# Kernel tuning notes

Measured on AMD Instinct MI355X. Metric: run time of the kernel, lower is better.

The kernel has to match this reference:

```python
import jax, jax.numpy as jnp
import numpy as np

N = 100000   # nodes
E = 1600000  # edges
G = 64       # graphs in batch
C = 8        # num_classes
H = 128      # hidden dim


def _lin(k, out_f, in_f):
    return jax.random.normal(k, (out_f, in_f), jnp.float32) * (1.0 / np.sqrt(in_f))


def setup_inputs() -> dict:
    key = jax.random.key(0)
    ks = jax.random.split(key, 16)
    x = jax.random.normal(ks[0], (N, 5), jnp.float32)
    edge_index = jax.random.randint(ks[1], (2, E), 0, N)
    batch = jnp.sort(jax.random.randint(ks[2], (N,), 0, G))
    exinfo = jax.random.normal(ks[3], (G, 10), jnp.float32)
    return {
        "x": x, "edge_index": edge_index, "batch": batch, "exinfo": exinfo,
        # GraphConv1: 3 -> 128 (PyG GraphConv: lin_root(x) + lin_rel(scatter_add(x_j)))
        "Wroot1": _lin(ks[4], H, 3), "Wrel1": _lin(ks[5], H, 3), "brel1": jnp.zeros((H,), jnp.float32),
        # GraphConv2: 128 -> 128
        "Wroot2": _lin(ks[6], H, H), "Wrel2": _lin(ks[7], H, H), "brel2": jnp.zeros((H,), jnp.float32),
        # MLP head
        "W1": _lin(ks[8], 64, 2 * H + 10), "b1": jnp.zeros((64,), jnp.float32),
        "W2": _lin(ks[9], 32, 64), "b2": jnp.zeros((32,), jnp.float32),
        "W3": _lin(ks[10], C, 32), "b3": jnp.zeros((C,), jnp.float32),
    }


def _graph_conv(x, src, dst, Wroot, Wrel, brel):
    # PyG GraphConv (aggr='add'): out_i = Wrel @ sum_{j->i} x_j + brel + Wroot @ x_i
    agg = jax.ops.segment_sum(x[src], dst, num_segments=x.shape[0])  # [N, F]
    return agg @ Wrel.T + brel + x @ Wroot.T


def reference(x, edge_index, batch, exinfo,
              Wroot1, Wrel1, brel1, Wroot2, Wrel2, brel2,
              W1, b1, W2, b2, W3, b3):
    xs = x[:, 2:5]                              # data.x[:, 2:5]
    src, dst = edge_index[0], edge_index[1]
    x1 = jax.nn.relu(_graph_conv(xs, src, dst, Wroot1, Wrel1, brel1))   # [N, 128]
    x2 = jax.nn.relu(_graph_conv(x1, src, dst, Wroot2, Wrel2, brel2))   # [N, 128]
    h = jnp.concatenate([x1, x2], axis=-1)      # [N, 256]
    g = jax.ops.segment_max(h, batch, num_segments=G)  # global max pool [G, 256]
    g = jnp.concatenate([g, exinfo], axis=-1)   # [G, 266]
    g = jax.nn.relu(g @ W1.T + b1)
    g = jax.nn.relu(g @ W2.T + b2)
    return jax.nn.log_softmax(g @ W3.T + b3, axis=-1)
```

## Files before the change

### kernel.cpp

```cpp
#include <hip/hip_runtime.h>

#define N_NODES 100000
#define N_EDGES 1600000
#define NG 64
#define NC 8
#define HD 128

#define BUCKET_SHIFT 8
#define NB ((N_NODES + 255) >> 8)
#define NCHUNK 256
#define EPC (N_EDGES / NCHUNK)

typedef __attribute__((ext_vector_type(8))) __bf16 bf16x8;
typedef __attribute__((ext_vector_type(4))) float f32x4;
typedef __attribute__((ext_vector_type(2))) float f32x2;


__global__ void hist_init_k(const int* __restrict__ dst, int* __restrict__ hist,
                            const float* __restrict__ x, const float* __restrict__ Wrel2,
                            const float* __restrict__ Wroot2, float4* __restrict__ xs4,
                            __bf16* __restrict__ Wc, unsigned int* __restrict__ g) {
  int t = threadIdx.x;
  if (blockIdx.x < NCHUNK) {
    __shared__ int lh[NB];
    int c = blockIdx.x;
    for (int b = t; b < NB; b += 256) lh[b] = 0;
    __syncthreads();
    int e0 = c * EPC;
    for (int i = t; i < EPC; i += 256) atomicAdd(&lh[dst[e0 + i] >> BUCKET_SHIFT], 1);
    __syncthreads();
    for (int b = t; b < NB; b += 256) hist[c * NB + b] = lh[b];
  } else {
    int i = (blockIdx.x - NCHUNK) * 256 + t;
    if (i < 64 * 256) g[i] = 0u;
    if (i < 32768) {
      int h = i >> 8, k = i & 255;
      float v = (k < 128) ? Wrel2[h * 128 + k] : Wroot2[h * 128 + (k - 128)];
      Wc[i] = (__bf16)v;
    }
    if (i < N_NODES) {
      const float* xp = x + (size_t)i * 5;
      xs4[i] = make_float4(xp[2], xp[3], xp[4], 0.f);
    }
  }
}


__launch_bounds__(512)
__global__ void sum_scan_k(const int* __restrict__ hist, int* __restrict__ bucket_base,
                           int* __restrict__ row_ptr) {
  __shared__ int sm[512];
  int t = threadIdx.x;
  int s = 0;
  if (t < NB) {
#pragma unroll 8
    for (int c = 0; c < NCHUNK; c++) s += hist[c * NB + t];
  }
  sm[t] = s;
  __syncthreads();
  for (int off = 1; off < 512; off <<= 1) {
    int v = (t >= off) ? sm[t - off] : 0;
    __syncthreads();
    sm[t] += v;
    __syncthreads();
  }
  if (t < NB) bucket_base[t] = sm[t] - s;
  if (t == 0) { bucket_base[NB] = N_EDGES; row_ptr[N_NODES] = N_EDGES; }
}

__global__ void chunk_scan_k(int* __restrict__ hist, const int* __restrict__ bucket_base) {
  int b = blockIdx.x, lane = threadIdx.x;
  int carry = bucket_base[b];
#pragma unroll
  for (int it = 0; it < NCHUNK / 64; it++) {
    int c = it * 64 + lane;
    int v = hist[c * NB + b];
    int s = v;
#pragma unroll
    for (int off = 1; off < 64; off <<= 1) {
      int u = __shfl_up(s, off);
      if (lane >= off) s += u;
    }
    hist[c * NB + b] = carry + s - v;
    carry += __shfl(s, 63);
  }
}

__global__ void scatter_k(const int* __restrict__ src, const int* __restrict__ dst,
                          const int* __restrict__ hist, unsigned int* __restrict__ pairs) {
  __shared__ int loff[NB];
  int c = blockIdx.x, t = threadIdx.x;
  for (int b = t; b < NB; b += 256) loff[b] = hist[c * NB + b];
  __syncthreads();
  int e0 = c * EPC;
  for (int i = t; i < EPC; i += 256) {
    int d = dst[e0 + i], s = src[e0 + i];
    int pos = atomicAdd(&loff[d >> BUCKET_SHIFT], 1);
    pairs[pos] = ((unsigned int)s << 8) | (unsigned int)(d & 255);
  }
}

__global__ void bucket_csr_k(const unsigned int* __restrict__ pairs,
                             const int* __restrict__ bucket_base,
                             int* __restrict__ row_ptr, int* __restrict__ csr) {
  __shared__ int cnt[256];
  __shared__ int start[256];
  __shared__ int wsum[4];
  int b = blockIdx.x, t = threadIdx.x, lane = t & 63, wid = t >> 6;
  int nb0 = b << BUCKET_SHIFT;
  int beg = bucket_base[b], end = bucket_base[b + 1];
  cnt[t] = 0;
  __syncthreads();
  for (int i = beg + t; i < end; i += 256) atomicAdd(&cnt[pairs[i] & 255u], 1);
  __syncthreads();
  int v = cnt[t];
  int s = v;
#pragma unroll
  for (int off = 1; off < 64; off <<= 1) {
    int u = __shfl_up(s, off);
    if (lane >= off) s += u;
  }
  if (lane == 63) wsum[wid] = s;
  __syncthreads();
  if (t == 0) {
    int a = 0;
    for (int j = 0; j < 4; j++) { int x = wsum[j]; wsum[j] = a; a += x; }
  }
  __syncthreads();
  int excl = wsum[wid] + s - v;
  start[t] = excl;
  if (nb0 + t < N_NODES) row_ptr[nb0 + t] = beg + excl;
  cnt[t] = 0;
  __syncthreads();
  for (int i = beg + t; i < end; i += 256) {
    unsigned int p = pairs[i];
    int li = p & 255u;
    int pos = beg + start[li] + atomicAdd(&cnt[li], 1);
    csr[pos] = (int)(p >> 8);
  }
}


__global__ void conv1_k(const float4* __restrict__ xs4, const int* __restrict__ row_ptr,
                        const int* __restrict__ csr, const float* __restrict__ Wroot1,
                        const float* __restrict__ Wrel1, const float* __restrict__ brel1,
                        __bf16* __restrict__ xcat) {
  int node = blockIdx.x * 4 + (threadIdx.x >> 6);
  if (node >= N_NODES) return;
  int lane = threadIdx.x & 63;
  int beg = row_ptr[node], end = row_ptr[node + 1];
  float a0 = 0.f, a1 = 0.f, a2 = 0.f;
  for (int e = beg + lane; e < end; e += 64) {
    float4 v = xs4[csr[e]];
    a0 += v.x; a1 += v.y; a2 += v.z;
  }
#pragma unroll
  for (int m = 1; m < 64; m <<= 1) {
    a0 += __shfl_xor(a0, m);
    a1 += __shfl_xor(a1, m);
    a2 += __shfl_xor(a2, m);
  }
  float4 rv = xs4[node];
  __bf16* orow = xcat + (size_t)node * 256 + 128;
#pragma unroll
  for (int hh = 0; hh < 2; hh++) {
    int h = lane + hh * 64;
    float v = brel1[h]
            + a0 * Wrel1[h * 3 + 0] + a1 * Wrel1[h * 3 + 1] + a2 * Wrel1[h * 3 + 2]
            + rv.x * Wroot1[h * 3 + 0] + rv.y * Wroot1[h * 3 + 1] + rv.z * Wroot1[h * 3 + 2];
    orow[h] = (__bf16)fmaxf(v, 0.f);
  }
}


#define LDROW(s) (*((const uint4*)(xcat + (size_t)(s) * 256 + 128) + f))
#define ACC8(u) \
  acc2[0] += (f32x2){__uint_as_float((u).x << 16), __uint_as_float((u).x & 0xffff0000u)}; \
  acc2[1] += (f32x2){__uint_as_float((u).y << 16), __uint_as_float((u).y & 0xffff0000u)}; \
  acc2[2] += (f32x2){__uint_as_float((u).z << 16), __uint_as_float((u).z & 0xffff0000u)}; \
  acc2[3] += (f32x2){__uint_as_float((u).w << 16), __uint_as_float((u).w & 0xffff0000u)};

__global__ void agg2_k(const int* __restrict__ row_ptr, const int* __restrict__ csr,
                       __bf16* xcat) {
  int node = blockIdx.x * 4 + (threadIdx.x >> 6);
  if (node >= N_NODES) return;
  int lane = threadIdx.x & 63;
  int g = lane >> 4, f = lane & 15;
  int beg = row_ptr[node], end = row_ptr[node + 1];
  int deg = end - beg;
  int idx = (lane < deg) ? csr[beg + lane] : 0;
  f32x2 acc2[4];
#pragma unroll
  for (int k = 0; k < 4; k++) acc2[k] = (f32x2){0.f, 0.f};
  int dmain = deg < 64 ? deg : 64;
  int j = 0;
  for (; j + 16 <= dmain; j += 16) {
    int s0 = __shfl(idx, j + g);
    int s1 = __shfl(idx, j + 4 + g);
    int s2 = __shfl(idx, j + 8 + g);
    int s3 = __shfl(idx, j + 12 + g);
    uint4 u0 = LDROW(s0);
    uint4 u1 = LDROW(s1);
    uint4 u2 = LDROW(s2);
    uint4 u3 = LDROW(s3);
    ACC8(u0) ACC8(u1) ACC8(u2) ACC8(u3)
  }
  if (j + 8 <= dmain) {
    int s0 = __shfl(idx, j + g);
    int s1 = __shfl(idx, j + 4 + g);
    uint4 u0 = LDROW(s0);
    uint4 u1 = LDROW(s1);
    ACC8(u0) ACC8(u1)
    j += 8;
  }
  if (j + 4 <= dmain) {
    int s0 = __shfl(idx, j + g);
    uint4 u0 = LDROW(s0);
    ACC8(u0)
    j += 4;
  }
  {
    int rem = dmain - j;
    int s0 = __shfl(idx, j + (g < rem ? g : 0));
    if (g < rem) {
      uint4 u0 = LDROW(s0);
      ACC8(u0)
    }
  }
  for (int e = beg + 64; e < end; e += 4) {
    int m = end - e;
    int s0 = csr[e + (g < m ? g : 0)];
    if (g < m) {
      uint4 u0 = LDROW(s0);
      ACC8(u0)
    }
  }
#pragma unroll
  for (int k = 0; k < 4; k++) {
    acc2[k].x += __shfl_xor(acc2[k].x, 16);
    acc2[k].y += __shfl_xor(acc2[k].y, 16);
    acc2[k].x += __shfl_xor(acc2[k].x, 32);
    acc2[k].y += __shfl_xor(acc2[k].y, 32);
  }
  if (g == 0) {
    uint4 o;
    o.x = (__float_as_uint((float)(__bf16)acc2[0].x) >> 16) | (__float_as_uint((float)(__bf16)acc2[0].y) & 0xffff0000u);
    o.y = (__float_as_uint((float)(__bf16)acc2[1].x) >> 16) | (__float_as_uint((float)(__bf16)acc2[1].y) & 0xffff0000u);
    o.z = (__float_as_uint((float)(__bf16)acc2[2].x) >> 16) | (__float_as_uint((float)(__bf16)acc2[2].y) & 0xffff0000u);
    o.w = (__float_as_uint((float)(__bf16)acc2[3].x) >> 16) | (__float_as_uint((float)(__bf16)acc2[3].y) & 0xffff0000u);
    *((uint4*)(xcat + (size_t)node * 256) + f) = o;
  }
}


__launch_bounds__(512, 4)
__global__ void gemm2_k(const __bf16* __restrict__ xcat, const __bf16* __restrict__ Wc,
                        const float* __restrict__ brel2, const int* __restrict__ batch,
                        unsigned int* __restrict__ gout) {
  __shared__ char Blds[128 * 256 * 2];
  int t = threadIdx.x;
  for (int i = t; i < 4096; i += 512) {
    uint4 v = ((const uint4*)Wc)[i];
    int byte = i * 16;
    int sw = byte ^ (((byte >> 9) & 7) << 4);
    *(uint4*)(Blds + sw) = v;
  }
  __syncthreads();
  int wid = t >> 6, lane = t & 63;
  int nb = (blockIdx.x * 8 + wid) * 32;
  if (nb >= N_NODES) return;
  int r = lane & 15, ko = lane >> 4;
  const __bf16* arow0 = xcat + (size_t)(nb + r) * 256 + ko * 8;
  const __bf16* arow1 = arow0 + 16 * 256;
  f32x4 acc0[8], acc1[8];
#pragma unroll
  for (int i = 0; i < 8; i++) {
    acc0[i] = (f32x4){0.f, 0.f, 0.f, 0.f};
    acc1[i] = (f32x4){0.f, 0.f, 0.f, 0.f};
  }
#pragma unroll
  for (int kb = 0; kb < 256; kb += 32) {
    bf16x8 a0 = *(const bf16x8*)(arow0 + kb);
    bf16x8 a1 = *(const bf16x8*)(arow1 + kb);
#pragma unroll
    for (int ht = 0; ht < 8; ht++) {
      int h = ht * 16 + r;
      int byte = h * 512 + ko * 16 + kb * 2;
      bf16x8 b = *(const bf16x8*)(Blds + (byte ^ ((r & 7) << 4)));
      acc0[ht] = __builtin_amdgcn_mfma_f32_16x16x32_bf16(a0, b, acc0[ht], 0, 0, 0);
      acc1[ht] = __builtin_amdgcn_mfma_f32_16x16x32_bf16(a1, b, acc1[ht], 0, 0, 0);
    }
  }
  int gfirst = batch[nb], glast = batch[nb + 31];
  if (gfirst == glast) {
    unsigned int* gp = gout + gfirst * 256 + 128;
#pragma unroll
    for (int ht = 0; ht < 8; ht++) {
      float bias = brel2[ht * 16 + r];
      float m = 0.f;
#pragma unroll
      for (int rr = 0; rr < 4; rr++) {
        m = fmaxf(m, acc0[ht][rr] + bias);
        m = fmaxf(m, acc1[ht][rr] + bias);
      }
      m = fmaxf(m, __shfl_xor(m, 16));
      m = fmaxf(m, __shfl_xor(m, 32));
      if (ko == 0) atomicMax(&gp[ht * 16 + r], __float_as_uint(m));
    }
  } else {
    int g0[4], g1[4];
#pragma unroll
    for (int rr = 0; rr < 4; rr++) {
      g0[rr] = batch[nb + ko * 4 + rr];
      g1[rr] = batch[nb + 16 + ko * 4 + rr];
    }
#pragma unroll
    for (int ht = 0; ht < 8; ht++) {
      int h = ht * 16 + r;
      float bias = brel2[h];
#pragma unroll
      for (int rr = 0; rr < 4; rr++) {
        atomicMax(&gout[g0[rr] * 256 + 128 + h],
                  __float_as_uint(fmaxf(acc0[ht][rr] + bias, 0.f)));
        atomicMax(&gout[g1[rr] * 256 + 128 + h],
                  __float_as_uint(fmaxf(acc1[ht][rr] + bias, 0.f)));
      }
    }
  }
}


__global__ void segmax1_k(const __bf16* __restrict__ xcat, const int* __restrict__ batch,
                          unsigned int* __restrict__ g) {
  int t = threadIdx.x;
  int f = t & 63;
  int s = t >> 6;
  int n0 = blockIdx.x * 256;
  float m0 = 0.f, m1 = 0.f;
  int cur = -1;
  int n1 = n0 + 256 < N_NODES ? n0 + 256 : N_NODES;
  for (int n = n0 + s; n < n1; n += 4) {
    int b = batch[n];
    if (b != cur) {
      if (cur >= 0) {
        atomicMax(&g[cur * 256 + 2 * f], __float_as_uint(m0));
        atomicMax(&g[cur * 256 + 2 * f + 1], __float_as_uint(m1));
      }
      cur = b; m0 = 0.f; m1 = 0.f;
    }
    unsigned int u = ((const unsigned int*)(xcat + (size_t)n * 256 + 128))[f];
    m0 = fmaxf(m0, __uint_as_float(u << 16));
    m1 = fmaxf(m1, __uint_as_float(u & 0xffff0000u));
  }
  if (cur >= 0) {
    atomicMax(&g[cur * 256 + 2 * f], __float_as_uint(m0));
    atomicMax(&g[cur * 256 + 2 * f + 1], __float_as_uint(m1));
  }
}


__global__ void head1_k(const float* __restrict__ g, const float* __restrict__ exinfo,
                        const float* __restrict__ W1, const float* __restrict__ b1,
                        float* __restrict__ g1) {
  int gg = blockIdx.x;
  int t = threadIdx.x;
  int c = t >> 2, q = t & 3;
  const float* w = W1 + c * 266;
  const float* gr = g + gg * 256;
  float s = 0.f;
  for (int k = q * 64; k < q * 64 + 64; k++) s += gr[k] * w[k];
  if (q == 0) {
    const float* er = exinfo + gg * 10;
    for (int k = 0; k < 10; k++) s += er[k] * w[256 + k];
    s += b1[c];
  }
  s += __shfl_xor(s, 1);
  s += __shfl_xor(s, 2);
  if (q == 0) g1[gg * 64 + c] = fmaxf(s, 0.f);
}

__global__ void head2_k(const float* __restrict__ g1, const float* __restrict__ W2,
                        const float* __restrict__ b2, const float* __restrict__ W3,
                        const float* __restrict__ b3, float* __restrict__ out) {
  __shared__ float s1[64 * 64];
  __shared__ float s2[64 * 32];
  int t = threadIdx.x;
  for (int i = t; i < 4096; i += 256) s1[i] = g1[i];
  __syncthreads();
  for (int o = t; o < 2048; o += 256) {
    int r = o >> 5, c = o & 31;
    float s = b2[c];
    for (int k = 0; k < 64; k++) s += s1[r * 64 + k] * W2[c * 64 + k];
    s2[r * 32 + c] = fmaxf(s, 0.f);
  }
  __syncthreads();
  if (t < 64) {
    float lg[8];
#pragma unroll
    for (int c = 0; c < 8; c++) {
      float s = b3[c];
      for (int k = 0; k < 32; k++) s += s2[t * 32 + k] * W3[c * 32 + k];
      lg[c] = s;
    }
    float mx = lg[0];
#pragma unroll
    for (int c = 1; c < 8; c++) mx = fmaxf(mx, lg[c]);
    float se = 0.f;
#pragma unroll
    for (int c = 0; c < 8; c++) se += expf(lg[c] - mx);
    float lse = mx + logf(se);
#pragma unroll
    for (int c = 0; c < 8; c++) out[t * 8 + c] = lg[c] - lse;
  }
}


extern "C" void kernel_launch(void* const* d_in, const int* in_sizes, int n_in,
                              void* d_out, int out_size, void* d_ws, size_t ws_size,
                              hipStream_t stream) {
  const float* x      = (const float*)d_in[0];
  const int*   edge   = (const int*)d_in[1];
  const int*   batch  = (const int*)d_in[2];
  const float* exinfo = (const float*)d_in[3];
  const float* Wroot1 = (const float*)d_in[4];
  const float* Wrel1  = (const float*)d_in[5];
  const float* brel1  = (const float*)d_in[6];
  const float* Wroot2 = (const float*)d_in[7];
  const float* Wrel2  = (const float*)d_in[8];
  const float* brel2  = (const float*)d_in[9];
  const float* W1     = (const float*)d_in[10];
  const float* b1     = (const float*)d_in[11];
  const float* W2     = (const float*)d_in[12];
  const float* b2     = (const float*)d_in[13];
  const float* W3     = (const float*)d_in[14];
  const float* b3     = (const float*)d_in[15];
  const int* src = edge;
  const int* dst = edge + N_EDGES;

  char* p = (char*)d_ws;
  auto alloc = [&](size_t bytes) {
    char* q = p;
    p += (bytes + 511) & ~(size_t)511;
    return (void*)q;
  };
  __bf16*       Wc          = (__bf16*)alloc(128 * 256 * 2);
  unsigned int* g           = (unsigned int*)alloc(64 * 256 * 4);
  float*        g1          = (float*)alloc(64 * 64 * 4);
  float4*       xs4         = (float4*)alloc((size_t)N_NODES * 16);
  int*          hist        = (int*)alloc((size_t)NCHUNK * NB * 4);
  int*          bucket_base = (int*)alloc((size_t)(NB + 1) * 4);
  int*          row_ptr     = (int*)alloc((size_t)(N_NODES + 1) * 4);
  int*          csr         = (int*)alloc((size_t)N_EDGES * 4);
  __bf16*       xcat        = (__bf16*)alloc((size_t)N_NODES * 256 * 2);
  unsigned int* pairs       = (unsigned int*)alloc((size_t)N_EDGES * 4);

  hist_init_k<<<NCHUNK + NB, 256, 0, stream>>>(dst, hist, x, Wrel2, Wroot2, xs4, Wc, g);
  sum_scan_k<<<1, 512, 0, stream>>>(hist, bucket_base, row_ptr);
  chunk_scan_k<<<NB, 64, 0, stream>>>(hist, bucket_base);
  scatter_k<<<NCHUNK, 256, 0, stream>>>(src, dst, hist, pairs);
  bucket_csr_k<<<NB, 256, 0, stream>>>(pairs, bucket_base, row_ptr, csr);
  conv1_k<<<25000, 256, 0, stream>>>(xs4, row_ptr, csr, Wroot1, Wrel1, brel1, xcat);
  agg2_k<<<25000, 256, 0, stream>>>(row_ptr, csr, xcat);
  gemm2_k<<<391, 512, 0, stream>>>(xcat, Wc, brel2, batch, g);
  segmax1_k<<<NB, 256, 0, stream>>>(xcat, batch, g);
  head1_k<<<64, 256, 0, stream>>>((const float*)g, exinfo, W1, b1, g1);
  head2_k<<<1, 256, 0, stream>>>(g1, W2, b2, W3, b3, (float*)d_out);
}
```

Baseline: 206.6 us.

## Fuse conv1 aggregation into CSR build and x1 max-pool into gemm2

The conv1 neighbour sum now accumulates per-bucket in shared memory with float atomics while the CSR is built, so the separate conv1 pass over the CSR goes away. The x1 global max pool is folded into gemm2, which already loads those xcat rows as MFMA operands, removing the segmax1 kernel. sum_scan is rewritten to spread the histogram reduction over all threads using LDS atomics. The trade-offs are more LDS atomic contention, an order-dependent float summation, and per-thread serial 128-wide output writes in the CSR kernel.

```diff
diff --git a/kernel.cpp b/kernel.cpp
--- a/kernel.cpp
+++ b/kernel.cpp
@@ -51,12 +51,14 @@
                            int* __restrict__ row_ptr) {
   __shared__ int sm[512];
   int t = threadIdx.x;
-  int s = 0;
-  if (t < NB) {
-#pragma unroll 8
-    for (int c = 0; c < NCHUNK; c++) s += hist[c * NB + t];
-  }
-  sm[t] = s;
+  sm[t] = 0;
+  __syncthreads();
+  for (int i = t; i < NCHUNK * NB; i += 512) {
+    int b = i - (i / NB) * NB;
+    atomicAdd(&sm[b], hist[i]);
+  }
+  __syncthreads();
+  int s = sm[t];
   __syncthreads();
   for (int off = 1; off < 512; off <<= 1) {
     int v = (t >= off) ? sm[t - off] : 0;
@@ -100,18 +102,33 @@
   }
 }
 
-__global__ void bucket_csr_k(const unsigned int* __restrict__ pairs,
-                             const int* __restrict__ bucket_base,
-                             int* __restrict__ row_ptr, int* __restrict__ csr) {
+
+__global__ void csr_conv1_k(const unsigned int* __restrict__ pairs,
+                            const int* __restrict__ bucket_base,
+                            const float4* __restrict__ xs4,
+                            const float* __restrict__ Wroot1, const float* __restrict__ Wrel1,
+                            const float* __restrict__ brel1,
+                            int* __restrict__ row_ptr, int* __restrict__ csr,
+                            __bf16* __restrict__ xcat) {
   __shared__ int cnt[256];
   __shared__ int start[256];
   __shared__ int wsum[4];
+  __shared__ float agg[256][3];
   int b = blockIdx.x, t = threadIdx.x, lane = t & 63, wid = t >> 6;
   int nb0 = b << BUCKET_SHIFT;
   int beg = bucket_base[b], end = bucket_base[b + 1];
   cnt[t] = 0;
-  __syncthreads();
-  for (int i = beg + t; i < end; i += 256) atomicAdd(&cnt[pairs[i] & 255u], 1);
+  agg[t][0] = 0.f; agg[t][1] = 0.f; agg[t][2] = 0.f;
+  __syncthreads();
+  for (int i = beg + t; i < end; i += 256) {
+    unsigned int p = pairs[i];
+    int li = p & 255u;
+    atomicAdd(&cnt[li], 1);
+    float4 v = xs4[p >> 8];
+    atomicAdd(&agg[li][0], v.x);
+    atomicAdd(&agg[li][1], v.y);
+    atomicAdd(&agg[li][2], v.z);
+  }
   __syncthreads();
   int v = cnt[t];
   int s = v;
@@ -138,37 +155,30 @@
     int pos = beg + start[li] + atomicAdd(&cnt[li], 1);
     csr[pos] = (int)(p >> 8);
   }
-}
-
-
-__global__ void conv1_k(const float4* __restrict__ xs4, const int* __restrict__ row_ptr,
-                        const int* __restrict__ csr, const float* __restrict__ Wroot1,
-                        const float* __restrict__ Wrel1, const float* __restrict__ brel1,
-                        __bf16* __restrict__ xcat) {
-  int node = blockIdx.x * 4 + (threadIdx.x >> 6);
-  if (node >= N_NODES) return;
-  int lane = threadIdx.x & 63;
-  int beg = row_ptr[node], end = row_ptr[node + 1];
-  float a0 = 0.f, a1 = 0.f, a2 = 0.f;
-  for (int e = beg + lane; e < end; e += 64) {
-    float4 v = xs4[csr[e]];
-    a0 += v.x; a1 += v.y; a2 += v.z;
-  }
-#pragma unroll
-  for (int m = 1; m < 64; m <<= 1) {
-    a0 += __shfl_xor(a0, m);
-    a1 += __shfl_xor(a1, m);
-    a2 += __shfl_xor(a2, m);
-  }
-  float4 rv = xs4[node];
-  __bf16* orow = xcat + (size_t)node * 256 + 128;
-#pragma unroll
-  for (int hh = 0; hh < 2; hh++) {
-    int h = lane + hh * 64;
-    float v = brel1[h]
-            + a0 * Wrel1[h * 3 + 0] + a1 * Wrel1[h * 3 + 1] + a2 * Wrel1[h * 3 + 2]
-            + rv.x * Wroot1[h * 3 + 0] + rv.y * Wroot1[h * 3 + 1] + rv.z * Wroot1[h * 3 + 2];
-    orow[h] = (__bf16)fmaxf(v, 0.f);
+  int node = nb0 + t;
+  if (node < N_NODES) {
+    float a0 = agg[t][0], a1 = agg[t][1], a2 = agg[t][2];
+    float4 rv = xs4[node];
+    uint4* orow = (uint4*)(xcat + (size_t)node * 256 + 128);
+#pragma unroll 4
+    for (int q = 0; q < 16; q++) {
+      unsigned int w[4];
+#pragma unroll
+      for (int d = 0; d < 4; d++) {
+        int h = q * 8 + d * 2;
+        float v0 = brel1[h]
+                 + a0 * Wrel1[h * 3 + 0] + a1 * Wrel1[h * 3 + 1] + a2 * Wrel1[h * 3 + 2]
+                 + rv.x * Wroot1[h * 3 + 0] + rv.y * Wroot1[h * 3 + 1] + rv.z * Wroot1[h * 3 + 2];
+        float v1 = brel1[h + 1]
+                 + a0 * Wrel1[h * 3 + 3] + a1 * Wrel1[h * 3 + 4] + a2 * Wrel1[h * 3 + 5]
+                 + rv.x * Wroot1[h * 3 + 3] + rv.y * Wroot1[h * 3 + 4] + rv.z * Wroot1[h * 3 + 5];
+        v0 = fmaxf(v0, 0.f);
+        v1 = fmaxf(v1, 0.f);
+        w[d] = (__float_as_uint((float)(__bf16)v0) >> 16) |
+               (__float_as_uint((float)(__bf16)v1) & 0xffff0000u);
+      }
+      orow[q] = make_uint4(w[0], w[1], w[2], w[3]);
+    }
   }
 }
 
@@ -270,6 +280,8 @@
   int nb = (blockIdx.x * 8 + wid) * 32;
   if (nb >= N_NODES) return;
   int r = lane & 15, ko = lane >> 4;
+  int gfirst = batch[nb], glast = batch[nb + 31];
+  bool fast = (gfirst == glast);
   const __bf16* arow0 = xcat + (size_t)(nb + r) * 256 + ko * 8;
   const __bf16* arow1 = arow0 + 16 * 256;
   f32x4 acc0[8], acc1[8];
@@ -282,17 +294,43 @@
   for (int kb = 0; kb < 256; kb += 32) {
     bf16x8 a0 = *(const bf16x8*)(arow0 + kb);
     bf16x8 a1 = *(const bf16x8*)(arow1 + kb);
+    if (kb >= 128) {
+      if (fast) {
+        float m[8];
+#pragma unroll
+        for (int j = 0; j < 8; j++) m[j] = fmaxf((float)a0[j], (float)a1[j]);
+#pragma unroll
+        for (int j = 0; j < 8; j++) {
+          m[j] = fmaxf(m[j], __shfl_xor(m[j], 1));
+          m[j] = fmaxf(m[j], __shfl_xor(m[j], 2));
+          m[j] = fmaxf(m[j], __shfl_xor(m[j], 4));
+          m[j] = fmaxf(m[j], __shfl_xor(m[j], 8));
+        }
+        if (r == 0) {
+#pragma unroll
+          for (int j = 0; j < 8; j++)
+            atomicMax(&gout[gfirst * 256 + (kb - 128) + ko * 8 + j], __float_as_uint(m[j]));
+        }
+      } else {
+        int ga = batch[nb + r], gb = batch[nb + 16 + r];
+#pragma unroll
+        for (int j = 0; j < 8; j++) {
+          int fo = (kb - 128) + ko * 8 + j;
+          atomicMax(&gout[ga * 256 + fo], __float_as_uint((float)a0[j]));
+          atomicMax(&gout[gb * 256 + fo], __float_as_uint((float)a1[j]));
+        }
+      }
+    }
 #pragma unroll
     for (int ht = 0; ht < 8; ht++) {
       int h = ht * 16 + r;
       int byte = h * 512 + ko * 16 + kb * 2;
-      bf16x8 b = *(const bf16x8*)(Blds + (byte ^ ((r & 7) << 4)));
-      acc0[ht] = __builtin_amdgcn_mfma_f32_16x16x32_bf16(a0, b, acc0[ht], 0, 0, 0);
-      acc1[ht] = __builtin_amdgcn_mfma_f32_16x16x32_bf16(a1, b, acc1[ht], 0, 0, 0);
-    }
-  }
-  int gfirst = batch[nb], glast = batch[nb + 31];
-  if (gfirst == glast) {
+      bf16x8 bfr = *(const bf16x8*)(Blds + (byte ^ ((r & 7) << 4)));
+      acc0[ht] = __builtin_amdgcn_mfma_f32_16x16x32_bf16(a0, bfr, acc0[ht], 0, 0, 0);
+      acc1[ht] = __builtin_amdgcn_mfma_f32_16x16x32_bf16(a1, bfr, acc1[ht], 0, 0, 0);
+    }
+  }
+  if (fast) {
     unsigned int* gp = gout + gfirst * 256 + 128;
 #pragma unroll
     for (int ht = 0; ht < 8; ht++) {
@@ -326,35 +364,6 @@
                   __float_as_uint(fmaxf(acc1[ht][rr] + bias, 0.f)));
       }
     }
-  }
-}
-
-
-__global__ void segmax1_k(const __bf16* __restrict__ xcat, const int* __restrict__ batch,
-                          unsigned int* __restrict__ g) {
-  int t = threadIdx.x;
-  int f = t & 63;
-  int s = t >> 6;
-  int n0 = blockIdx.x * 256;
-  float m0 = 0.f, m1 = 0.f;
-  int cur = -1;
-  int n1 = n0 + 256 < N_NODES ? n0 + 256 : N_NODES;
-  for (int n = n0 + s; n < n1; n += 4) {
-    int b = batch[n];
-    if (b != cur) {
-      if (cur >= 0) {
-        atomicMax(&g[cur * 256 + 2 * f], __float_as_uint(m0));
-        atomicMax(&g[cur * 256 + 2 * f + 1], __float_as_uint(m1));
-      }
-      cur = b; m0 = 0.f; m1 = 0.f;
-    }
-    unsigned int u = ((const unsigned int*)(xcat + (size_t)n * 256 + 128))[f];
-    m0 = fmaxf(m0, __uint_as_float(u << 16));
-    m1 = fmaxf(m1, __uint_as_float(u & 0xffff0000u));
-  }
-  if (cur >= 0) {
-    atomicMax(&g[cur * 256 + 2 * f], __float_as_uint(m0));
-    atomicMax(&g[cur * 256 + 2 * f + 1], __float_as_uint(m1));
   }
 }
 
@@ -458,11 +467,10 @@
   sum_scan_k<<<1, 512, 0, stream>>>(hist, bucket_base, row_ptr);
   chunk_scan_k<<<NB, 64, 0, stream>>>(hist, bucket_base);
   scatter_k<<<NCHUNK, 256, 0, stream>>>(src, dst, hist, pairs);
-  bucket_csr_k<<<NB, 256, 0, stream>>>(pairs, bucket_base, row_ptr, csr);
-  conv1_k<<<25000, 256, 0, stream>>>(xs4, row_ptr, csr, Wroot1, Wrel1, brel1, xcat);
+  csr_conv1_k<<<NB, 256, 0, stream>>>(pairs, bucket_base, xs4, Wroot1, Wrel1, brel1,
+                                      row_ptr, csr, xcat);
   agg2_k<<<25000, 256, 0, stream>>>(row_ptr, csr, xcat);
   gemm2_k<<<391, 512, 0, stream>>>(xcat, Wc, brel2, batch, g);
-  segmax1_k<<<NB, 256, 0, stream>>>(xcat, batch, g);
   head1_k<<<64, 256, 0, stream>>>((const float*)g, exinfo, W1, b1, g1);
   head2_k<<<1, 256, 0, stream>>>(g1, W2, b2, W3, b3, (float*)d_out);
 }
```

Result: slower. 315.3 us (+52.7%).
